# Kernel optimization log

Measured on AMD Instinct MI355X. Metric: run time of the kernel, lower is better.

## Reference

```python
import jax, jax.numpy as jnp
import numpy as np

N = 20000   # nodes
E = 40000   # directed edges
F_IN = 13   # dataset.num_features
G = 1000    # graphs in batch
DIMS = [(13, 32), (32, 64), (64, 64)]  # (M_in, M_out) per NNConv layer


def setup_inputs() -> dict:
    key = jax.random.key(0)
    ks = list(jax.random.split(key, 32))
    inp = {}
    inp["x"] = jax.random.normal(ks[0], (N, F_IN), jnp.float32)
    inp["edge_index"] = jax.random.randint(ks[1], (2, E), 0, N, dtype=jnp.int32)
    inp["edge_attr"] = jax.random.uniform(ks[2], (E, 5), dtype=jnp.float32)
    inp["batch"] = jnp.sort(jax.random.randint(ks[3], (N,), 0, G, dtype=jnp.int32))
    i = 4
    for l, (mi, mo) in enumerate(DIMS):
        inp[f"w1_{l}"] = jax.random.normal(ks[i], (5, 128), jnp.float32) / np.sqrt(5.0).astype(np.float32); i += 1
        inp[f"b1_{l}"] = jnp.zeros((128,), jnp.float32)
        inp[f"w2_{l}"] = jax.random.normal(ks[i], (128, mi * mo), jnp.float32) / np.sqrt(128.0).astype(np.float32); i += 1
        inp[f"b2_{l}"] = jnp.zeros((mi * mo,), jnp.float32)
        inp[f"root_{l}"] = jax.random.normal(ks[i], (mi, mo), jnp.float32) / np.sqrt(float(mi)).astype(np.float32); i += 1
        inp[f"bias_{l}"] = jnp.zeros((mo,), jnp.float32)
    inp["fc1_w"] = jax.random.normal(ks[i], (64, 32), jnp.float32) / 8.0; i += 1
    inp["fc1_b"] = jnp.zeros((32,), jnp.float32)
    inp["fc2_w"] = jax.random.normal(ks[i], (32, 16), jnp.float32) / np.sqrt(32.0).astype(np.float32); i += 1
    inp["fc2_b"] = jnp.zeros((16,), jnp.float32)
    inp["fc3_w"] = jax.random.normal(ks[i], (16, 1), jnp.float32) / 4.0; i += 1
    inp["fc3_b"] = jnp.zeros((1,), jnp.float32)
    return inp


def _nnconv(x, src, dst, edge_attr, w1, b1, w2, b2, root, bias, mi, mo):
    # edge MLP: [E,5] -> [E,128] -> [E, mi*mo] per-edge weight matrices
    h = jax.nn.relu(edge_attr @ w1 + b1)
    We = (h @ w2 + b2).reshape(-1, mi, mo)          # [E, mi, mo]
    msg = jnp.einsum('ei,eio->eo', x[src], We)      # gather + per-edge matmul
    agg = jax.ops.segment_sum(msg, dst, num_segments=x.shape[0])  # scatter-add
    return x @ root + agg + bias                    # NNConv root weight + bias


def _forward(x, edge_index, edge_attr, batch, convs, fc1_w, fc1_b, fc2_w, fc2_b, fc3_w, fc3_b):
    src, dst = edge_index[0], edge_index[1]
    for (mi, mo), (w1, b1, w2, b2, root, bias) in zip(DIMS, convs):
        x = jax.nn.elu(_nnconv(x, src, dst, edge_attr, w1, b1, w2, b2, root, bias, mi, mo))
    # scatter_mean pooling over graphs
    sums = jax.ops.segment_sum(x, batch, num_segments=G)
    cnt = jax.ops.segment_sum(jnp.ones((x.shape[0],), x.dtype), batch, num_segments=G)
    xg = sums / jnp.maximum(cnt, 1.0)[:, None]
    xg = jax.nn.elu(xg @ fc1_w + fc1_b)
    xg = jax.nn.elu(xg @ fc2_w + fc2_b)
    return (xg @ fc3_w + fc3_b).reshape(-1)


def reference(x, edge_index, edge_attr, batch,
              w1_0, b1_0, w2_0, b2_0, root_0, bias_0,
              w1_1, b1_1, w2_1, b2_1, root_1, bias_1,
              w1_2, b1_2, w2_2, b2_2, root_2, bias_2,
              fc1_w, fc1_b, fc2_w, fc2_b, fc3_w, fc3_b):
    convs = [(w1_0, b1_0, w2_0, b2_0, root_0, bias_0),
             (w1_1, b1_1, w2_1, b2_1, root_1, bias_1),
             (w1_2, b1_2, w2_2, b2_2, root_2, bias_2)]
    return _forward(x, edge_index, edge_attr, batch, convs,
                    fc1_w, fc1_b, fc2_w, fc2_b, fc3_w, fc3_b)
```

## Files before the change

### kernel.cpp

```cpp
#include <hip/hip_runtime.h>
#include <stdint.h>
#include <math.h>

typedef _Float16 half8_t __attribute__((ext_vector_type(8)));
typedef float floatx4 __attribute__((ext_vector_type(4)));

#define NN 20000
#define NE 40000
#define NG 1000
#define NBLK 313
#define NSPLIT 4

__global__ __launch_bounds__(256) void prep_all_kernel(
    const float* __restrict__ w2a, const float* __restrict__ b2a, _Float16* __restrict__ oa,
    const float* __restrict__ w2b, const float* __restrict__ b2b, _Float16* __restrict__ ob,
    const float* __restrict__ w2c, const float* __restrict__ b2c, _Float16* __restrict__ oc)
{
  const int TOT0 = 68 * 2 * 64, TOT1 = 132 * 4 * 64, TOT2 = 264 * 4 * 64;
  int idx = blockIdx.x * 256 + threadIdx.x;
  const float *w2, *b2; _Float16* op; int mi, mo, mpsh, CT;
  if (idx < TOT0) { w2 = w2a; b2 = b2a; op = oa; mi = 13; mo = 32; mpsh = 4; CT = 2; }
  else if (idx < TOT0 + TOT1) { idx -= TOT0; w2 = w2b; b2 = b2b; op = ob; mi = 32; mo = 64; mpsh = 5; CT = 4; }
  else if (idx < TOT0 + TOT1 + TOT2) { idx -= TOT0 + TOT1; w2 = w2c; b2 = b2c; op = oc; mi = 64; mo = 64; mpsh = 6; CT = 4; }
  else return;
  int l = idx & 63;
  int ct = (idx >> 6) % CT;
  int c = idx / (64 * CT);
  int q = l >> 4;
  int n = ct * 16 + (l & 15);
  int mask = (1 << mpsh) - 1;
  half8_t v;
#pragma unroll
  for (int j = 0; j < 8; ++j) {
    int r = c * 32 + q * 8 + j;
    int k = r >> mpsh, i = r & mask;
    float f = 0.f;
    if (i < mi) {
      if (k < 128) f = w2[(size_t)(k * mi + i) * mo + n];
      else if (k == 128) f = b2[(size_t)i * mo + n];
    }
    v[j] = (_Float16)f;
  }
  *(half8_t*)(op + (size_t)idx * 8) = v;
}

__global__ __launch_bounds__(256) void prep0_kernel(
    const float* __restrict__ x, const float* __restrict__ root,
    const float* __restrict__ bias, _Float16* __restrict__ e16,
    float* __restrict__ xn0)
{
  __shared__ float xs[8 * 13];
  int n0 = blockIdx.x * 8;
  int t = threadIdx.x;
  if (t < 104) xs[t] = x[(size_t)n0 * 13 + t];
  __syncthreads();
  if (t < 128) {
    int r = t >> 4, i = t & 15;
    e16[(size_t)(n0 + r) * 16 + i] = (i < 13) ? (_Float16)xs[r * 13 + i] : (_Float16)0.f;
  }
  int r = t >> 5, o = t & 31;
  float acc = bias[o];
#pragma unroll
  for (int i = 0; i < 13; ++i) acc = fmaf(xs[r * 13 + i], root[i * 32 + o], acc);
  xn0[(size_t)(n0 + r) * 32 + o] = acc;
}

template <int MI, int MOX>
__global__ __launch_bounds__(256) void elu_root_kernel(
    const float* __restrict__ xin, const float* __restrict__ root,
    const float* __restrict__ bias, _Float16* __restrict__ e16,
    float* __restrict__ xnext)
{
  constexpr int R = 256 / MOX;
  __shared__ float es[R * MI];
  int n0 = blockIdx.x * R;
  int t = threadIdx.x;
  for (int idx = t; idx < R * MI; idx += 256) {
    float v = xin[(size_t)n0 * MI + idx];
    v = v > 0.f ? v : (expf(v) - 1.f);
    es[idx] = v;
    e16[(size_t)n0 * MI + idx] = (_Float16)v;
  }
  __syncthreads();
  int r = t / MOX, o = t % MOX;
  float acc = bias[o];
#pragma unroll 8
  for (int i = 0; i < MI; ++i) acc = fmaf(es[r * MI + i], root[i * MOX + o], acc);
  xnext[(size_t)(n0 + r) * MOX + o] = acc;
}

template <int MIP, int MO, int NCC, int KCNT>
__global__ __launch_bounds__(256, 4) void msg7_kernel(
    const float* __restrict__ ea, const float* __restrict__ w1,
    const float* __restrict__ b1, const _Float16* __restrict__ xe,
    const int* __restrict__ src, const int* __restrict__ dst,
    const _Float16* __restrict__ w2h, float* __restrict__ xn)
{
  constexpr int CT = MO / 16;
  constexpr int CHB = CT * 1024;
  constexpr int XLSS = MIP + 8;
  constexpr int HSTW = KCNT | 1;
  constexpr int XV = (MIP == 64) ? 2 : 1;
  constexpr int NU2 = MIP / 16;
  constexpr int KH = (KCNT + 1) >> 1;
  constexpr int XB = 128 * XLSS * 2;
  constexpr int HB = 128 * HSTW * 4;
  constexpr int SBYTES = (XB > HB) ? XB : HB;

  __shared__ char sb[SBYTES];
  __shared__ uint4 wsb[2][CHB / 16];
  __shared__ float w1s[5 * 128 + 128];
  __shared__ int dsts[128];

  _Float16* sxb = (_Float16*)sb;
  unsigned* hls = (unsigned*)sb;

  const int t = threadIdx.x;
  const int wave = t >> 6, lane = t & 63;
  const int l15 = lane & 15, q = lane >> 4;
  const int split = blockIdx.x / NBLK;
  const int e0 = (blockIdx.x % NBLK) * 128;
  const int c0 = NCC * split;
  const int kg0 = KCNT * split;

  {
    int rowA = t >> 1;
    int egA = e0 + rowA; if (egA >= NE) egA = NE - 1;
    const uint4* xr = (const uint4*)(xe + (size_t)src[egA] * MIP);
    uint4* xd = (uint4*)(sxb + rowA * XLSS);
#pragma unroll
    for (int u = 0; u < NU2; ++u) xd[(t & 1) * NU2 + u] = xr[(t & 1) * NU2 + u];
  }
  if (t < 128) {
    int eg = e0 + t; if (eg >= NE) eg = NE - 1;
    dsts[t] = dst[eg];
  }
  const int te = t & 127;
  float ear[5];
  {
    int ege = e0 + te; if (ege >= NE) ege = NE - 1;
#pragma unroll
    for (int j = 0; j < 5; ++j) ear[j] = ea[(size_t)ege * 5 + j];
  }
  for (int i = t; i < 768; i += 256) w1s[i] = (i < 640) ? w1[i] : b1[i - 640];
  __syncthreads();

  const int wbase = wave * 32;
  half8_t xf[2][XV];
#pragma unroll
  for (int s = 0; s < 2; ++s) {
    int el = wbase + s * 16 + l15;
    int i0 = (MIP == 16) ? (q & 1) * 8 : q * 8;
    xf[s][0] = *(const half8_t*)(sxb + el * XLSS + i0);
    if constexpr (MIP == 64)
      xf[s][XV - 1] = *(const half8_t*)(sxb + el * XLSS + 32 + q * 8);
  }
  __syncthreads();

  {
    int kh = t >> 7;
    int klo = kh * KH;
    int khi = klo + KH; if (khi > KCNT) khi = KCNT;
    for (int kl = klo; kl < khi; ++kl) {
      int kg = kg0 + kl;
      float v;
      if (kg < 128) {
        v = w1s[640 + kg];
#pragma unroll
        for (int j = 0; j < 5; ++j) v = fmaf(ear[j], w1s[j * 128 + kg], v);
        v = fmaxf(v, 0.f);
      } else v = (kg == 128) ? 1.f : 0.f;
      union { _Float16 f; unsigned short u; } cv; cv.f = (_Float16)v;
      hls[te * HSTW + kl] = (unsigned)cv.u * 0x10001u;
    }
  }
  __syncthreads();

  floatx4 acc[2][CT];
#pragma unroll
  for (int s = 0; s < 2; ++s)
#pragma unroll
    for (int b = 0; b < CT; ++b) acc[s][b] = (floatx4){0.f, 0.f, 0.f, 0.f};

  const char* wgp = (const char*)w2h + (size_t)c0 * CHB;
  uint4 r4; uint2 r2;
  if constexpr (CT == 4) r4 = *(const uint4*)(wgp + t * 16);
  else r2 = *(const uint2*)(wgp + t * 8);

#pragma unroll 2
  for (int cc = 0; cc < NCC; ++cc) {
    if constexpr (CT == 4) wsb[cc & 1][t] = r4;
    else ((uint2*)wsb[cc & 1])[t] = r2;
    __syncthreads();
    if (cc + 1 < NCC) {
      if constexpr (CT == 4) r4 = *(const uint4*)(wgp + (size_t)(cc + 1) * CHB + t * 16);
      else r2 = *(const uint2*)(wgp + (size_t)(cc + 1) * CHB + t * 8);
    }
    const _Float16* wb = (const _Float16*)wsb[cc & 1];
    half8_t bf[CT];
#pragma unroll
    for (int b = 0; b < CT; ++b)
      bf[b] = *(const half8_t*)(wb + (b * 64 + lane) * 8);
    int kl;
    if constexpr (MIP == 64) kl = cc >> 1;
    else if constexpr (MIP == 32) kl = cc;
    else kl = 2 * cc + (q >> 1);
#pragma unroll
    for (int s = 0; s < 2; ++s) {
      _Float16 hv = *(const _Float16*)(hls + (wbase + s * 16 + l15) * HSTW + kl);
      half8_t af;
      if constexpr (MIP == 64) af = xf[s][cc & 1] * hv;
      else af = xf[s][0] * hv;
#pragma unroll
      for (int b = 0; b < CT; ++b)
        acc[s][b] = __builtin_amdgcn_mfma_f32_16x16x32_f16(af, bf[b], acc[s][b], 0, 0, 0);
    }
  }

#pragma unroll
  for (int s = 0; s < 2; ++s) {
    int rowb = wbase + s * 16 + q * 4;
#pragma unroll
    for (int b = 0; b < CT; ++b) {
      int n = b * 16 + l15;
#pragma unroll
      for (int r = 0; r < 4; ++r) {
        int row = rowb + r;
        if (e0 + row < NE)
          atomicAdd(&xn[(size_t)dsts[row] * MO + n], acc[s][b][r]);
      }
    }
  }
}

__global__ __launch_bounds__(64) void pool_fc_kernel(
    const float* __restrict__ xn2, const int* __restrict__ batch,
    const float* __restrict__ f1w, const float* __restrict__ f1b,
    const float* __restrict__ f2w, const float* __restrict__ f2b,
    const float* __restrict__ f3w, const float* __restrict__ f3b,
    float* __restrict__ out)
{
  __shared__ float xg[64]; __shared__ float a1[32]; __shared__ float a2[16];
  int g = blockIdx.x, t = threadIdx.x;
  int lo = 0, hi = NN;
  while (lo < hi) { int m = (lo + hi) >> 1; if (batch[m] < g) lo = m + 1; else hi = m; }
  int start = lo; hi = NN;
  while (lo < hi) { int m = (lo + hi) >> 1; if (batch[m] <= g) lo = m + 1; else hi = m; }
  int end = lo;
  float acc = 0.f;
  for (int n = start; n < end; ++n) {
    float v = xn2[(size_t)n * 64 + t];
    acc += v > 0.f ? v : (expf(v) - 1.f);
  }
  float c = (end > start) ? (float)(end - start) : 1.f;
  xg[t] = acc / c;
  __syncthreads();
  if (t < 32) {
    float a = f1b[t];
    for (int i = 0; i < 64; ++i) a = fmaf(xg[i], f1w[i * 32 + t], a);
    a1[t] = a > 0.f ? a : (expf(a) - 1.f);
  }
  __syncthreads();
  if (t < 16) {
    float a = f2b[t];
    for (int i = 0; i < 32; ++i) a = fmaf(a1[i], f2w[i * 16 + t], a);
    a2[t] = a > 0.f ? a : (expf(a) - 1.f);
  }
  __syncthreads();
  if (t == 0) {
    float a = f3b[0];
    for (int i = 0; i < 16; ++i) a = fmaf(a2[i], f3w[i], a);
    out[g] = a;
  }
}

extern "C" void kernel_launch(void* const* d_in, const int* in_sizes, int n_in,
                              void* d_out, int out_size, void* d_ws, size_t ws_size,
                              hipStream_t stream)
{
  const float* x_in  = (const float*)d_in[0];
  const int*   ei    = (const int*)d_in[1];
  const float* ea    = (const float*)d_in[2];
  const int*   batch = (const int*)d_in[3];
  const float* W1[3] = {(const float*)d_in[4],  (const float*)d_in[10], (const float*)d_in[16]};
  const float* B1[3] = {(const float*)d_in[5],  (const float*)d_in[11], (const float*)d_in[17]};
  const float* W2[3] = {(const float*)d_in[6],  (const float*)d_in[12], (const float*)d_in[18]};
  const float* B2[3] = {(const float*)d_in[7],  (const float*)d_in[13], (const float*)d_in[19]};
  const float* RT[3] = {(const float*)d_in[8],  (const float*)d_in[14], (const float*)d_in[20]};
  const float* BS[3] = {(const float*)d_in[9],  (const float*)d_in[15], (const float*)d_in[21]};
  const float* f1w = (const float*)d_in[22]; const float* f1b = (const float*)d_in[23];
  const float* f2w = (const float*)d_in[24]; const float* f2b = (const float*)d_in[25];
  const float* f3w = (const float*)d_in[26]; const float* f3b = (const float*)d_in[27];

  char* ws = (char*)d_ws;
  size_t off = 0;
  auto alloc = [&](size_t bytes) { void* p = ws + off; off += (bytes + 255) & ~(size_t)255; return p; };
  float*    xn0   = (float*)alloc((size_t)NN * 32 * 4);
  float*    xn1   = (float*)alloc((size_t)NN * 64 * 4);
  float*    xn2   = (float*)alloc((size_t)NN * 64 * 4);
  _Float16* e16_0 = (_Float16*)alloc((size_t)NN * 16 * 2);
  _Float16* e16_1 = (_Float16*)alloc((size_t)NN * 32 * 2);
  _Float16* e16_2 = (_Float16*)alloc((size_t)NN * 64 * 2);
  _Float16* w2h0  = (_Float16*)alloc((size_t)68 * 2048);
  _Float16* w2h1  = (_Float16*)alloc((size_t)132 * 4096);
  _Float16* w2h2  = (_Float16*)alloc((size_t)264 * 4096);

  const int* srcp = ei;
  const int* dstp = ei + NE;

  prep_all_kernel<<<(68*2*64 + 132*4*64 + 264*4*64 + 255) / 256, 256, 0, stream>>>(
      W2[0], B2[0], w2h0, W2[1], B2[1], w2h1, W2[2], B2[2], w2h2);
  prep0_kernel<<<NN / 8, 256, 0, stream>>>(x_in, RT[0], BS[0], e16_0, xn0);

  msg7_kernel<16, 32, 17, 34><<<NBLK * NSPLIT, 256, 0, stream>>>(
      ea, W1[0], B1[0], e16_0, srcp, dstp, w2h0, xn0);
  elu_root_kernel<32, 64><<<NN / 4, 256, 0, stream>>>(xn0, RT[1], BS[1], e16_1, xn1);

  msg7_kernel<32, 64, 33, 33><<<NBLK * NSPLIT, 256, 0, stream>>>(
      ea, W1[1], B1[1], e16_1, srcp, dstp, w2h1, xn1);
  elu_root_kernel<64, 64><<<NN / 4, 256, 0, stream>>>(xn1, RT[2], BS[2], e16_2, xn2);

  msg7_kernel<64, 64, 66, 33><<<NBLK * NSPLIT, 256, 0, stream>>>(
      ea, W1[2], B1[2], e16_2, srcp, dstp, w2h2, xn2);

  pool_fc_kernel<<<NG, 64, 0, stream>>>(xn2, batch, f1w, f1b, f2w, f2b, f3w, f3b, (float*)d_out);
}
```

Baseline: 305.0 us.

## Fuse prep kernels, preload edge-MLP scalars to registers, deepen weight prefetch

Merges the layer-0 node prep kernel into the weight-repacking kernel so one launch does both jobs. In the message kernel, the per-edge hidden scalars are stored as 16-bit values and packed two per register ahead of the MFMA loop, which removes LDS reads from the inner loop. The loop is now fully unrolled with a two-deep register prefetch of weight chunks, and launch bounds drop to 3 blocks per SM. The cost is higher register pressure and lower occupancy in exchange for less LDS traffic and more latency hiding.

```diff
diff --git a/kernel.cpp b/kernel.cpp
--- a/kernel.cpp
+++ b/kernel.cpp
@@ -11,13 +11,32 @@
 #define NBLK 313
 #define NSPLIT 4
 
-__global__ __launch_bounds__(256) void prep_all_kernel(
+__global__ __launch_bounds__(256) void prep_fused_kernel(
+    const float* __restrict__ x, const float* __restrict__ root0,
+    const float* __restrict__ bias0, _Float16* __restrict__ e16, float* __restrict__ xn0,
     const float* __restrict__ w2a, const float* __restrict__ b2a, _Float16* __restrict__ oa,
     const float* __restrict__ w2b, const float* __restrict__ b2b, _Float16* __restrict__ ob,
     const float* __restrict__ w2c, const float* __restrict__ b2c, _Float16* __restrict__ oc)
 {
+  if (blockIdx.x < 2500) {
+    __shared__ float xs[8 * 13];
+    int n0 = blockIdx.x * 8;
+    int t = threadIdx.x;
+    if (t < 104) xs[t] = x[(size_t)n0 * 13 + t];
+    __syncthreads();
+    if (t < 128) {
+      int r = t >> 4, i = t & 15;
+      e16[(size_t)(n0 + r) * 16 + i] = (i < 13) ? (_Float16)xs[r * 13 + i] : (_Float16)0.f;
+    }
+    int r = t >> 5, o = t & 31;
+    float acc = bias0[o];
+#pragma unroll
+    for (int i = 0; i < 13; ++i) acc = fmaf(xs[r * 13 + i], root0[i * 32 + o], acc);
+    xn0[(size_t)(n0 + r) * 32 + o] = acc;
+    return;
+  }
   const int TOT0 = 68 * 2 * 64, TOT1 = 132 * 4 * 64, TOT2 = 264 * 4 * 64;
-  int idx = blockIdx.x * 256 + threadIdx.x;
+  int idx = (blockIdx.x - 2500) * 256 + threadIdx.x;
   const float *w2, *b2; _Float16* op; int mi, mo, mpsh, CT;
   if (idx < TOT0) { w2 = w2a; b2 = b2a; op = oa; mi = 13; mo = 32; mpsh = 4; CT = 2; }
   else if (idx < TOT0 + TOT1) { idx -= TOT0; w2 = w2b; b2 = b2b; op = ob; mi = 32; mo = 64; mpsh = 5; CT = 4; }
@@ -44,27 +63,6 @@
   *(half8_t*)(op + (size_t)idx * 8) = v;
 }
 
-__global__ __launch_bounds__(256) void prep0_kernel(
-    const float* __restrict__ x, const float* __restrict__ root,
-    const float* __restrict__ bias, _Float16* __restrict__ e16,
-    float* __restrict__ xn0)
-{
-  __shared__ float xs[8 * 13];
-  int n0 = blockIdx.x * 8;
-  int t = threadIdx.x;
-  if (t < 104) xs[t] = x[(size_t)n0 * 13 + t];
-  __syncthreads();
-  if (t < 128) {
-    int r = t >> 4, i = t & 15;
-    e16[(size_t)(n0 + r) * 16 + i] = (i < 13) ? (_Float16)xs[r * 13 + i] : (_Float16)0.f;
-  }
-  int r = t >> 5, o = t & 31;
-  float acc = bias[o];
-#pragma unroll
-  for (int i = 0; i < 13; ++i) acc = fmaf(xs[r * 13 + i], root[i * 32 + o], acc);
-  xn0[(size_t)(n0 + r) * 32 + o] = acc;
-}
-
 template <int MI, int MOX>
 __global__ __launch_bounds__(256) void elu_root_kernel(
     const float* __restrict__ xin, const float* __restrict__ root,
@@ -89,8 +87,8 @@
   xnext[(size_t)(n0 + r) * MOX + o] = acc;
 }
 
-template <int MIP, int MO, int NCC, int KCNT>
-__global__ __launch_bounds__(256, 4) void msg7_kernel(
+template <int MIP, int MO, int NCC, int KREG, int KSTORE>
+__global__ __launch_bounds__(256, 3) void msg8_kernel(
     const float* __restrict__ ea, const float* __restrict__ w1,
     const float* __restrict__ b1, const _Float16* __restrict__ xe,
     const int* __restrict__ src, const int* __restrict__ dst,
@@ -99,12 +97,12 @@
   constexpr int CT = MO / 16;
   constexpr int CHB = CT * 1024;
   constexpr int XLSS = MIP + 8;
-  constexpr int HSTW = KCNT | 1;
+  constexpr int HST = KSTORE | 1;
   constexpr int XV = (MIP == 64) ? 2 : 1;
   constexpr int NU2 = MIP / 16;
-  constexpr int KH = (KCNT + 1) >> 1;
+  constexpr int KH = (KSTORE + 1) >> 1;
   constexpr int XB = 128 * XLSS * 2;
-  constexpr int HB = 128 * HSTW * 4;
+  constexpr int HB = 128 * HST * 2;
   constexpr int SBYTES = (XB > HB) ? XB : HB;
 
   __shared__ char sb[SBYTES];
@@ -113,7 +111,7 @@
   __shared__ int dsts[128];
 
   _Float16* sxb = (_Float16*)sb;
-  unsigned* hls = (unsigned*)sb;
+  unsigned short* hls = (unsigned short*)sb;
 
   const int t = threadIdx.x;
   const int wave = t >> 6, lane = t & 63;
@@ -121,7 +119,7 @@
   const int split = blockIdx.x / NBLK;
   const int e0 = (blockIdx.x % NBLK) * 128;
   const int c0 = NCC * split;
-  const int kg0 = KCNT * split;
+  const int kg0 = KSTORE * split;
 
   {
     int rowA = t >> 1;
@@ -155,12 +153,21 @@
     if constexpr (MIP == 64)
       xf[s][XV - 1] = *(const half8_t*)(sxb + el * XLSS + 32 + q * 8);
   }
+  const char* wgp = (const char*)w2h + (size_t)c0 * CHB;
+  uint4 rr4[2]; uint2 rr2[2];
+  if constexpr (CT == 4) {
+    rr4[0] = *(const uint4*)(wgp + t * 16);
+    rr4[1] = *(const uint4*)(wgp + CHB + t * 16);
+  } else {
+    rr2[0] = *(const uint2*)(wgp + t * 8);
+    rr2[1] = *(const uint2*)(wgp + CHB + t * 8);
+  }
   __syncthreads();
 
   {
     int kh = t >> 7;
     int klo = kh * KH;
-    int khi = klo + KH; if (khi > KCNT) khi = KCNT;
+    int khi = klo + KH; if (khi > KSTORE) khi = KSTORE;
     for (int kl = klo; kl < khi; ++kl) {
       int kg = kg0 + kl;
       float v;
@@ -171,10 +178,19 @@
         v = fmaxf(v, 0.f);
       } else v = (kg == 128) ? 1.f : 0.f;
       union { _Float16 f; unsigned short u; } cv; cv.f = (_Float16)v;
-      hls[te * HSTW + kl] = (unsigned)cv.u * 0x10001u;
-    }
-  }
-  __syncthreads();
+      hls[te * HST + kl] = cv.u;
+    }
+  }
+  __syncthreads();
+
+  unsigned hpk[KREG];
+#pragma unroll
+  for (int j = 0; j < KREG; ++j) {
+    int kl = (MIP == 16) ? (2 * j + (q >> 1)) : j;
+    unsigned lo = hls[(wbase + l15) * HST + kl];
+    unsigned hi = hls[(wbase + 16 + l15) * HST + kl];
+    hpk[j] = lo | (hi << 16);
+  }
 
   floatx4 acc[2][CT];
 #pragma unroll
@@ -182,38 +198,36 @@
 #pragma unroll
     for (int b = 0; b < CT; ++b) acc[s][b] = (floatx4){0.f, 0.f, 0.f, 0.f};
 
-  const char* wgp = (const char*)w2h + (size_t)c0 * CHB;
-  uint4 r4; uint2 r2;
-  if constexpr (CT == 4) r4 = *(const uint4*)(wgp + t * 16);
-  else r2 = *(const uint2*)(wgp + t * 8);
-
-#pragma unroll 2
+#pragma unroll
   for (int cc = 0; cc < NCC; ++cc) {
-    if constexpr (CT == 4) wsb[cc & 1][t] = r4;
-    else ((uint2*)wsb[cc & 1])[t] = r2;
+    if constexpr (CT == 4) wsb[cc & 1][t] = rr4[cc & 1];
+    else ((uint2*)wsb[cc & 1])[t] = rr2[cc & 1];
     __syncthreads();
-    if (cc + 1 < NCC) {
-      if constexpr (CT == 4) r4 = *(const uint4*)(wgp + (size_t)(cc + 1) * CHB + t * 16);
-      else r2 = *(const uint2*)(wgp + (size_t)(cc + 1) * CHB + t * 8);
+    {
+      int cp = (cc + 2 < NCC) ? (cc + 2) : cc;
+      if constexpr (CT == 4) rr4[cc & 1] = *(const uint4*)(wgp + (size_t)cp * CHB + t * 16);
+      else rr2[cc & 1] = *(const uint2*)(wgp + (size_t)cp * CHB + t * 8);
     }
     const _Float16* wb = (const _Float16*)wsb[cc & 1];
     half8_t bf[CT];
 #pragma unroll
     for (int b = 0; b < CT; ++b)
       bf[b] = *(const half8_t*)(wb + (b * 64 + lane) * 8);
-    int kl;
-    if constexpr (MIP == 64) kl = cc >> 1;
-    else if constexpr (MIP == 32) kl = cc;
-    else kl = 2 * cc + (q >> 1);
-#pragma unroll
-    for (int s = 0; s < 2; ++s) {
-      _Float16 hv = *(const _Float16*)(hls + (wbase + s * 16 + l15) * HSTW + kl);
-      half8_t af;
-      if constexpr (MIP == 64) af = xf[s][cc & 1] * hv;
-      else af = xf[s][0] * hv;
-#pragma unroll
-      for (int b = 0; b < CT; ++b)
-        acc[s][b] = __builtin_amdgcn_mfma_f32_16x16x32_f16(af, bf[b], acc[s][b], 0, 0, 0);
+
+    const int KI = (MIP == 64) ? (cc >> 1) : cc;
+    union { unsigned u; _Float16 f[2]; } uu; uu.u = hpk[KI];
+    half8_t af0, af1;
+    if constexpr (MIP == 64) {
+      af0 = xf[0][cc & 1] * uu.f[0];
+      af1 = xf[1][cc & 1] * uu.f[1];
+    } else {
+      af0 = xf[0][0] * uu.f[0];
+      af1 = xf[1][0] * uu.f[1];
+    }
+#pragma unroll
+    for (int b = 0; b < CT; ++b) {
+      acc[0][b] = __builtin_amdgcn_mfma_f32_16x16x32_f16(af0, bf[b], acc[0][b], 0, 0, 0);
+      acc[1][b] = __builtin_amdgcn_mfma_f32_16x16x32_f16(af1, bf[b], acc[1][b], 0, 0, 0);
     }
   }
 
@@ -308,19 +322,20 @@
   const int* srcp = ei;
   const int* dstp = ei + NE;
 
-  prep_all_kernel<<<(68*2*64 + 132*4*64 + 264*4*64 + 255) / 256, 256, 0, stream>>>(
+  const int PREPB = 2500 + (68*2*64 + 132*4*64 + 264*4*64 + 255) / 256;
+  prep_fused_kernel<<<PREPB, 256, 0, stream>>>(
+      x_in, RT[0], BS[0], e16_0, xn0,
       W2[0], B2[0], w2h0, W2[1], B2[1], w2h1, W2[2], B2[2], w2h2);
-  prep0_kernel<<<NN / 8, 256, 0, stream>>>(x_in, RT[0], BS[0], e16_0, xn0);
-
-  msg7_kernel<16, 32, 17, 34><<<NBLK * NSPLIT, 256, 0, stream>>>(
+
+  msg8_kernel<16, 32, 17, 17, 34><<<NBLK * NSPLIT, 256, 0, stream>>>(
       ea, W1[0], B1[0], e16_0, srcp, dstp, w2h0, xn0);
   elu_root_kernel<32, 64><<<NN / 4, 256, 0, stream>>>(xn0, RT[1], BS[1], e16_1, xn1);
 
-  msg7_kernel<32, 64, 33, 33><<<NBLK * NSPLIT, 256, 0, stream>>>(
+  msg8_kernel<32, 64, 33, 33, 33><<<NBLK * NSPLIT, 256, 0, stream>>>(
       ea, W1[1], B1[1], e16_1, srcp, dstp, w2h1, xn1);
   elu_root_kernel<64, 64><<<NN / 4, 256, 0, stream>>>(xn1, RT[2], BS[2], e16_2, xn2);
 
-  msg7_kernel<64, 64, 66, 33><<<NBLK * NSPLIT, 256, 0, stream>>>(
+  msg8_kernel<64, 64, 66, 33, 33><<<NBLK * NSPLIT, 256, 0, stream>>>(
       ea, W1[2], B1[2], e16_2, srcp, dstp, w2h2, xn2);
 
   pool_fc_kernel<<<NG, 64, 0, stream>>>(xn2, batch, f1w, f1b, f2w, f2b, f3w, f3b, (float*)d_out);
```

Result: slower. 367.0 us (+20.3%).

## Replace atomic scatter-add with CSR gather over per-split fp16 message buffers

Applied to the files above, without the earlier changes.

The message kernels now write per-edge, per-split fp16 messages to a scratch buffer instead of doing float atomicAdd into node features. A CSR (degree count, single-block scan, fill) is built by destination, and a gather kernel sums messages per node, fusing the root matmul, bias and ELU. This removes atomic contention and fuses the root/ELU passes. In exchange it adds several extra launches, including a serial single-block scan, an extra write and read of messages, and fp16 rounding of messages before summation.

```diff
diff --git a/kernel.cpp b/kernel.cpp
--- a/kernel.cpp
+++ b/kernel.cpp
@@ -11,13 +11,26 @@
 #define NBLK 313
 #define NSPLIT 4
 
-__global__ __launch_bounds__(256) void prep_all_kernel(
+__global__ __launch_bounds__(256) void prep_fused_kernel(
+    const float* __restrict__ x, _Float16* __restrict__ e16,
     const float* __restrict__ w2a, const float* __restrict__ b2a, _Float16* __restrict__ oa,
     const float* __restrict__ w2b, const float* __restrict__ b2b, _Float16* __restrict__ ob,
-    const float* __restrict__ w2c, const float* __restrict__ b2c, _Float16* __restrict__ oc)
-{
+    const float* __restrict__ w2c, const float* __restrict__ b2c, _Float16* __restrict__ oc,
+    int* __restrict__ deg)
+{
+  if (blockIdx.x < 1250) {
+    int idx = blockIdx.x * 256 + threadIdx.x;
+    int n = idx >> 4, i = idx & 15;
+    e16[idx] = (i < 13) ? (_Float16)x[(size_t)n * 13 + i] : (_Float16)0.f;
+    return;
+  }
+  if (blockIdx.x >= 1680) {
+    int n = (blockIdx.x - 1680) * 256 + threadIdx.x;
+    if (n < NN) deg[n] = 0;
+    return;
+  }
   const int TOT0 = 68 * 2 * 64, TOT1 = 132 * 4 * 64, TOT2 = 264 * 4 * 64;
-  int idx = blockIdx.x * 256 + threadIdx.x;
+  int idx = (blockIdx.x - 1250) * 256 + threadIdx.x;
   const float *w2, *b2; _Float16* op; int mi, mo, mpsh, CT;
   if (idx < TOT0) { w2 = w2a; b2 = b2a; op = oa; mi = 13; mo = 32; mpsh = 4; CT = 2; }
   else if (idx < TOT0 + TOT1) { idx -= TOT0; w2 = w2b; b2 = b2b; op = ob; mi = 32; mo = 64; mpsh = 5; CT = 4; }
@@ -44,57 +57,45 @@
   *(half8_t*)(op + (size_t)idx * 8) = v;
 }
 
-__global__ __launch_bounds__(256) void prep0_kernel(
-    const float* __restrict__ x, const float* __restrict__ root,
-    const float* __restrict__ bias, _Float16* __restrict__ e16,
-    float* __restrict__ xn0)
-{
-  __shared__ float xs[8 * 13];
-  int n0 = blockIdx.x * 8;
+__global__ __launch_bounds__(256) void deg_kernel(const int* __restrict__ dst, int* __restrict__ deg) {
+  int e = blockIdx.x * 256 + threadIdx.x;
+  if (e < NE) atomicAdd(&deg[dst[e]], 1);
+}
+
+__global__ __launch_bounds__(256) void scan_kernel(
+    const int* __restrict__ deg, int* __restrict__ row_ptr, int* __restrict__ cursor)
+{
+  __shared__ int ps[256];
   int t = threadIdx.x;
-  if (t < 104) xs[t] = x[(size_t)n0 * 13 + t];
-  __syncthreads();
-  if (t < 128) {
-    int r = t >> 4, i = t & 15;
-    e16[(size_t)(n0 + r) * 16 + i] = (i < 13) ? (_Float16)xs[r * 13 + i] : (_Float16)0.f;
-  }
-  int r = t >> 5, o = t & 31;
-  float acc = bias[o];
-#pragma unroll
-  for (int i = 0; i < 13; ++i) acc = fmaf(xs[r * 13 + i], root[i * 32 + o], acc);
-  xn0[(size_t)(n0 + r) * 32 + o] = acc;
-}
-
-template <int MI, int MOX>
-__global__ __launch_bounds__(256) void elu_root_kernel(
-    const float* __restrict__ xin, const float* __restrict__ root,
-    const float* __restrict__ bias, _Float16* __restrict__ e16,
-    float* __restrict__ xnext)
-{
-  constexpr int R = 256 / MOX;
-  __shared__ float es[R * MI];
-  int n0 = blockIdx.x * R;
-  int t = threadIdx.x;
-  for (int idx = t; idx < R * MI; idx += 256) {
-    float v = xin[(size_t)n0 * MI + idx];
-    v = v > 0.f ? v : (expf(v) - 1.f);
-    es[idx] = v;
-    e16[(size_t)n0 * MI + idx] = (_Float16)v;
-  }
-  __syncthreads();
-  int r = t / MOX, o = t % MOX;
-  float acc = bias[o];
-#pragma unroll 8
-  for (int i = 0; i < MI; ++i) acc = fmaf(es[r * MI + i], root[i * MOX + o], acc);
-  xnext[(size_t)(n0 + r) * MOX + o] = acc;
+  const int CH = (NN + 255) / 256;
+  int base = t * CH;
+  int s = 0;
+  for (int i = 0; i < CH; ++i) { int n = base + i; if (n < NN) s += deg[n]; }
+  ps[t] = s;
+  __syncthreads();
+  if (t == 0) { int run = 0; for (int i = 0; i < 256; ++i) { int v = ps[i]; ps[i] = run; run += v; } }
+  __syncthreads();
+  int run = ps[t];
+  for (int i = 0; i < CH; ++i) {
+    int n = base + i;
+    if (n < NN) { row_ptr[n] = run; cursor[n] = run; run += deg[n]; }
+    else if (n == NN) row_ptr[NN] = run;
+  }
+}
+
+__global__ __launch_bounds__(256) void fill_kernel(
+    const int* __restrict__ dst, int* __restrict__ cursor, int* __restrict__ eids)
+{
+  int e = blockIdx.x * 256 + threadIdx.x;
+  if (e < NE) { int p = atomicAdd(&cursor[dst[e]], 1); eids[p] = e; }
 }
 
 template <int MIP, int MO, int NCC, int KCNT>
-__global__ __launch_bounds__(256, 4) void msg7_kernel(
+__global__ __launch_bounds__(256, 4) void msg9_kernel(
     const float* __restrict__ ea, const float* __restrict__ w1,
     const float* __restrict__ b1, const _Float16* __restrict__ xe,
-    const int* __restrict__ src, const int* __restrict__ dst,
-    const _Float16* __restrict__ w2h, float* __restrict__ xn)
+    const int* __restrict__ src,
+    const _Float16* __restrict__ w2h, _Float16* __restrict__ msgp)
 {
   constexpr int CT = MO / 16;
   constexpr int CHB = CT * 1024;
@@ -110,7 +111,6 @@
   __shared__ char sb[SBYTES];
   __shared__ uint4 wsb[2][CHB / 16];
   __shared__ float w1s[5 * 128 + 128];
-  __shared__ int dsts[128];
 
   _Float16* sxb = (_Float16*)sb;
   unsigned* hls = (unsigned*)sb;
@@ -130,10 +130,6 @@
     uint4* xd = (uint4*)(sxb + rowA * XLSS);
 #pragma unroll
     for (int u = 0; u < NU2; ++u) xd[(t & 1) * NU2 + u] = xr[(t & 1) * NU2 + u];
-  }
-  if (t < 128) {
-    int eg = e0 + t; if (eg >= NE) eg = NE - 1;
-    dsts[t] = dst[eg];
   }
   const int te = t & 127;
   float ear[5];
@@ -217,6 +213,7 @@
     }
   }
 
+  _Float16* mp = msgp + (size_t)split * NE * MO;
 #pragma unroll
   for (int s = 0; s < 2; ++s) {
     int rowb = wbase + s * 16 + q * 4;
@@ -226,10 +223,40 @@
 #pragma unroll
       for (int r = 0; r < 4; ++r) {
         int row = rowb + r;
-        if (e0 + row < NE)
-          atomicAdd(&xn[(size_t)dsts[row] * MO + n], acc[s][b][r]);
+        int e = e0 + row;
+        if (e < NE) mp[(size_t)e * MO + n] = (_Float16)acc[s][b][r];
       }
     }
+  }
+}
+
+template <int MIN_, int XST, int MO, int FINAL>
+__global__ __launch_bounds__(256) void gather_kernel(
+    const _Float16* __restrict__ e16in, const float* __restrict__ root,
+    const float* __restrict__ bias, const int* __restrict__ row_ptr,
+    const int* __restrict__ eids, const _Float16* __restrict__ msgp,
+    _Float16* __restrict__ oute, float* __restrict__ outf)
+{
+  constexpr int NPB = 256 / MO;
+  int n = blockIdx.x * NPB + threadIdx.x / MO;
+  int o = threadIdx.x % MO;
+  if (n >= NN) return;
+  float a = bias[o];
+#pragma unroll
+  for (int i = 0; i < MIN_; ++i)
+    a = fmaf((float)e16in[(size_t)n * XST + i], root[i * MO + o], a);
+  int r0 = row_ptr[n], r1 = row_ptr[n + 1];
+  for (int j = r0; j < r1; ++j) {
+    int e = eids[j];
+#pragma unroll
+    for (int s = 0; s < NSPLIT; ++s)
+      a += (float)msgp[((size_t)s * NE + e) * MO + o];
+  }
+  if constexpr (FINAL) {
+    outf[(size_t)n * MO + o] = a;
+  } else {
+    float v = a > 0.f ? a : (expf(a) - 1.f);
+    oute[(size_t)n * MO + o] = (_Float16)v;
   }
 }
 
@@ -295,8 +322,6 @@
   char* ws = (char*)d_ws;
   size_t off = 0;
   auto alloc = [&](size_t bytes) { void* p = ws + off; off += (bytes + 255) & ~(size_t)255; return p; };
-  float*    xn0   = (float*)alloc((size_t)NN * 32 * 4);
-  float*    xn1   = (float*)alloc((size_t)NN * 64 * 4);
   float*    xn2   = (float*)alloc((size_t)NN * 64 * 4);
   _Float16* e16_0 = (_Float16*)alloc((size_t)NN * 16 * 2);
   _Float16* e16_1 = (_Float16*)alloc((size_t)NN * 32 * 2);
@@ -304,24 +329,35 @@
   _Float16* w2h0  = (_Float16*)alloc((size_t)68 * 2048);
   _Float16* w2h1  = (_Float16*)alloc((size_t)132 * 4096);
   _Float16* w2h2  = (_Float16*)alloc((size_t)264 * 4096);
+  _Float16* msgp  = (_Float16*)alloc((size_t)NSPLIT * NE * 64 * 2);
+  int*      deg     = (int*)alloc((size_t)NN * 4);
+  int*      row_ptr = (int*)alloc((size_t)(NN + 1) * 4);
+  int*      cursor  = (int*)alloc((size_t)NN * 4);
+  int*      eids    = (int*)alloc((size_t)NE * 4);
 
   const int* srcp = ei;
   const int* dstp = ei + NE;
 
-  prep_all_kernel<<<(68*2*64 + 132*4*64 + 264*4*64 + 255) / 256, 256, 0, stream>>>(
-      W2[0], B2[0], w2h0, W2[1], B2[1], w2h1, W2[2], B2[2], w2h2);
-  prep0_kernel<<<NN / 8, 256, 0, stream>>>(x_in, RT[0], BS[0], e16_0, xn0);
-
-  msg7_kernel<16, 32, 17, 34><<<NBLK * NSPLIT, 256, 0, stream>>>(
-      ea, W1[0], B1[0], e16_0, srcp, dstp, w2h0, xn0);
-  elu_root_kernel<32, 64><<<NN / 4, 256, 0, stream>>>(xn0, RT[1], BS[1], e16_1, xn1);
-
-  msg7_kernel<32, 64, 33, 33><<<NBLK * NSPLIT, 256, 0, stream>>>(
-      ea, W1[1], B1[1], e16_1, srcp, dstp, w2h1, xn1);
-  elu_root_kernel<64, 64><<<NN / 4, 256, 0, stream>>>(xn1, RT[2], BS[2], e16_2, xn2);
-
-  msg7_kernel<64, 64, 66, 33><<<NBLK * NSPLIT, 256, 0, stream>>>(
-      ea, W1[2], B1[2], e16_2, srcp, dstp, w2h2, xn2);
+  prep_fused_kernel<<<1680 + (NN + 255) / 256, 256, 0, stream>>>(
+      x_in, e16_0, W2[0], B2[0], w2h0, W2[1], B2[1], w2h1, W2[2], B2[2], w2h2, deg);
+  deg_kernel<<<(NE + 255) / 256, 256, 0, stream>>>(dstp, deg);
+  scan_kernel<<<1, 256, 0, stream>>>(deg, row_ptr, cursor);
+  fill_kernel<<<(NE + 255) / 256, 256, 0, stream>>>(dstp, cursor, eids);
+
+  msg9_kernel<16, 32, 17, 34><<<NBLK * NSPLIT, 256, 0, stream>>>(
+      ea, W1[0], B1[0], e16_0, srcp, w2h0, msgp);
+  gather_kernel<13, 16, 32, 0><<<(NN + 7) / 8, 256, 0, stream>>>(
+      e16_0, RT[0], BS[0], row_ptr, eids, msgp, e16_1, xn2);
+
+  msg9_kernel<32, 64, 33, 33><<<NBLK * NSPLIT, 256, 0, stream>>>(
+      ea, W1[1], B1[1], e16_1, srcp, w2h1, msgp);
+  gather_kernel<32, 32, 64, 0><<<(NN + 3) / 4, 256, 0, stream>>>(
+      e16_1, RT[1], BS[1], row_ptr, eids, msgp, e16_2, xn2);
+
+  msg9_kernel<64, 64, 66, 33><<<NBLK * NSPLIT, 256, 0, stream>>>(
+      ea, W1[2], B1[2], e16_2, srcp, w2h2, msgp);
+  gather_kernel<64, 64, 64, 1><<<(NN + 3) / 4, 256, 0, stream>>>(
+      e16_2, RT[2], BS[2], row_ptr, eids, msgp, e16_2, xn2);
 
   pool_fc_kernel<<<NG, 64, 0, stream>>>(xn2, batch, f1w, f1b, f2w, f2b, f3w, f3b, (float*)d_out);
 }
```

New measurement: 333.0 us. +9.2%, slower.
